# Performance work log

Measured on AMD Instinct MI355X. Metric: run time of the kernel, lower is better.

## Reference

```python
import jax, jax.numpy as jnp
import numpy as np

H = 12  # num_heads

def setup_inputs() -> dict:
    key = jax.random.key(0)
    ks = jax.random.split(key, 6)
    B, L, D = 2, 2048, 768
    x = jax.random.normal(ks[0], (B, L, D), dtype=jnp.float32)
    token_sizes = jax.random.uniform(ks[1], (B, L), dtype=jnp.float32)
    attn_mask = jnp.triu(jnp.ones((L, L), dtype=bool), k=1)
    key_padding_mask = jnp.zeros((B, L), dtype=bool)
    qkv_w = jax.random.normal(ks[2], (3 * D, D), dtype=jnp.float32) * (D ** -0.5)
    qkv_b = jax.random.normal(ks[3], (3 * D,), dtype=jnp.float32) * 0.02
    proj_w = jax.random.normal(ks[4], (D, D), dtype=jnp.float32) * (D ** -0.5)
    proj_b = jax.random.normal(ks[5], (D,), dtype=jnp.float32) * 0.02
    return {"x": x, "token_sizes": token_sizes, "attn_mask": attn_mask,
            "key_padding_mask": key_padding_mask, "qkv_w": qkv_w, "qkv_b": qkv_b,
            "proj_w": proj_w, "proj_b": proj_b}

def reference(x, token_sizes, attn_mask, key_padding_mask, qkv_w, qkv_b, proj_w, proj_b):
    B, L, D = x.shape
    hd = D // H
    scale = hd ** -0.5
    qkv = (x @ qkv_w.T + qkv_b).reshape(B, L, 3, H, hd)
    qkv = jnp.transpose(qkv, (2, 0, 3, 1, 4))  # [3, B, H, L, hd]
    q, k, v = qkv[0], qkv[1], qkv[2]
    logits = jnp.einsum('bhqd,bhkd->bhqk', q, k) * scale  # [B,H,L,L]
    neg = jnp.finfo(logits.dtype).min
    logits = jnp.where(attn_mask[None, None, :, :], neg, logits)
    logits = jnp.where(key_padding_mask[:, None, None, :], neg, logits)
    logits = logits + jnp.log(jnp.clip(token_sizes, 1e-8))[:, None, None, :]
    attn = jax.nn.softmax(logits, axis=-1)
    out = jnp.einsum('bhqk,bhkd->bhqd', attn, v)
    out = jnp.transpose(out, (0, 2, 1, 3)).reshape(B, L, D)
    out = out @ proj_w.T + proj_b
    k_merge = k.mean(axis=1)  # [B, L, hd]
    return (out, k_merge)
```

## Files before the change

### kernel.cpp

```cpp
#include <hip/hip_runtime.h>
#include <hip/hip_bf16.h>

typedef unsigned short u16;
typedef __bf16 bf16x8 __attribute__((ext_vector_type(8)));
typedef float f32x4 __attribute__((ext_vector_type(4)));

#define QSCALE (0.125f * 1.44269504088896340736f)

__device__ __forceinline__ u16 f2bf(float f) {
    __hip_bfloat16 h = __float2bfloat16(f);
    return __builtin_bit_cast(u16, h);
}
__device__ __forceinline__ float bf2f(u16 u) {
    unsigned int x = ((unsigned int)u) << 16;
    return __builtin_bit_cast(float, x);
}
__device__ __forceinline__ bf16x8 ld_bf8(const u16* p) {
    uint4 u = *reinterpret_cast<const uint4*>(p);
    return __builtin_bit_cast(bf16x8, u);
}
__device__ __forceinline__ bf16x8 pack8f(f32x4 a, f32x4 b) {
    union { bf16x8 v; u16 u[8]; } r;
    #pragma unroll
    for (int i = 0; i < 4; i++) { r.u[i] = f2bf(a[i]); r.u[4+i] = f2bf(b[i]); }
    return r.v;
}
__device__ __forceinline__ bf16x8 pack8u(ushort4 a, ushort4 b) {
    union { bf16x8 v; ushort4 u[2]; } r;
    r.u[0] = a; r.u[1] = b;
    return r.v;
}

#define GLOAD_LDS16(g, l) __builtin_amdgcn_global_load_lds( \
    (const __attribute__((address_space(1))) unsigned int*)(g), \
    (__attribute__((address_space(3))) unsigned int*)(l), 16, 0, 0)

template<int N> __device__ __forceinline__ void s_wait_vmcnt() {
    if constexpr (N == 0)       asm volatile("s_waitcnt vmcnt(0)" ::: "memory");
    else if constexpr (N == 3)  asm volatile("s_waitcnt vmcnt(3)" ::: "memory");
    else if constexpr (N == 4)  asm volatile("s_waitcnt vmcnt(4)" ::: "memory");
}
__device__ __forceinline__ void s_bar() {
    __builtin_amdgcn_sched_barrier(0);
    __builtin_amdgcn_s_barrier();
    __builtin_amdgcn_sched_barrier(0);
}
__device__ __forceinline__ void s_wait_lgkm0_bar() {
    asm volatile("s_waitcnt lgkmcnt(0)" ::: "memory");
    __builtin_amdgcn_sched_barrier(0);
    __builtin_amdgcn_s_barrier();
    __builtin_amdgcn_sched_barrier(0);
}

__global__ __launch_bounds__(256) void prep_kernel(
    const float* __restrict__ x, const float* __restrict__ qkvw,
    const float* __restrict__ projw, const float* __restrict__ ts,
    const unsigned char* __restrict__ kpm,
    u16* __restrict__ Xb, u16* __restrict__ Wq, u16* __restrict__ Wp,
    float* __restrict__ tsw, u16* __restrict__ tbf, int* __restrict__ qarr)
{
    int i = blockIdx.x * 256 + threadIdx.x;
    const int XC4 = 4096 * 768 / 4;
    const int WQ4 = 2304 * 768 / 4;
    const int WP4 = 768 * 768 / 4;
    const float* src = nullptr; u16* dst = nullptr;
    if (i < XC4) { src = x; dst = Xb; }
    else {
        i -= XC4;
        if (i < WQ4) { src = qkvw; dst = Wq; }
        else {
            i -= WQ4;
            if (i < WP4) { src = projw; dst = Wp; }
            else {
                i -= WP4;
                if (i < 1024) {
                    float4 t = *(const float4*)(ts + i*4);
                    uchar4 k = *(const uchar4*)(kpm + i*4);
                    float4 r;
                    r.x = k.x ? 0.f : fmaxf(t.x, 1e-8f);
                    r.y = k.y ? 0.f : fmaxf(t.y, 1e-8f);
                    r.z = k.z ? 0.f : fmaxf(t.z, 1e-8f);
                    r.w = k.w ? 0.f : fmaxf(t.w, 1e-8f);
                    *(float4*)(tsw + i*4) = r;
                    ushort4 o;
                    o.x = f2bf(r.x); o.y = f2bf(r.y);
                    o.z = f2bf(r.z); o.w = f2bf(r.w);
                    *(ushort4*)(tbf + i*4) = o;
                    return;
                }
                i -= 1024;
                if (i < 256) qarr[i] = 0;
                return;
            }
        }
    }
    float4 v = *(const float4*)(src + i*4);
    ushort4 o;
    o.x = f2bf(v.x); o.y = f2bf(v.y); o.z = f2bf(v.z); o.w = f2bf(v.w);
    *(ushort4*)(dst + i*4) = o;
}

template<int EPI, int MI>
__global__ __launch_bounds__(256, 2) void gemm_bt(
    const u16* __restrict__ A, const u16* __restrict__ Bm,
    const float* __restrict__ bias, const float* __restrict__ tsw,
    u16* __restrict__ Qb, u16* __restrict__ Kb, u16* __restrict__ Vt,
    float* __restrict__ outp)
{
    constexpr int BM = MI * 32;
    constexpr int ACALLS = MI / 2;
    constexpr int SA = ACALLS + 2;
    constexpr int NT = 24;
    __shared__ u16 As[2][BM * 32];
    __shared__ u16 Bs[2][128 * 32];
    const int K = 768;
    const int tid = threadIdx.x;
    const int nwg = gridDim.x * gridDim.y;
    const int flat = blockIdx.y * gridDim.x + blockIdx.x;
    const int per = nwg >> 3;
    const int swz = (flat & 7) * per + (flat >> 3);
    const int m0 = (swz / gridDim.x) * BM;
    const int n0 = (swz % gridDim.x) * 128;
    const int w = tid >> 6, lane = tid & 63;
    const int wr = (w >> 1) * (MI * 16), wc = (w & 1) * 64;
    const int g = lane >> 4, l16 = lane & 15;

    const int srow = lane >> 2;
    const int scol = (lane & 3) * 8;
    const u16* gA[ACALLS];
    #pragma unroll
    for (int c = 0; c < ACALLS; c++)
        gA[c] = A + (size_t)(m0 + (c*4 + w)*16 + srow) * K + scol;
    const u16* gB[2];
    #pragma unroll
    for (int c = 0; c < 2; c++)
        gB[c] = Bm + (size_t)(n0 + (c*4 + w)*16 + srow) * K + scol;

#define GSTAGE(buf, kk) do { \
    _Pragma("unroll") \
    for (int c = 0; c < ACALLS; c++) \
        GLOAD_LDS16(gA[c] + (kk), &As[buf][(c*4 + w) * 512]); \
    _Pragma("unroll") \
    for (int c = 0; c < 2; c++) \
        GLOAD_LDS16(gB[c] + (kk), &Bs[buf][(c*4 + w) * 512]); } while (0)

    f32x4 acc[MI][4] = {};
    GSTAGE(0, 0);
    GSTAGE(1, 32);
    for (int it = 0; it < NT; it++) {
        const int k0 = it * 32;
        const int cur = it & 1;
        if (it < NT - 1) s_wait_vmcnt<SA>();
        else             s_wait_vmcnt<0>();
        s_bar();
        bf16x8 af[MI], bfr[4];
        #pragma unroll
        for (int i = 0; i < MI; i++) af[i]  = ld_bf8(&As[cur][(wr + i*16 + l16)*32 + g*8]);
        #pragma unroll
        for (int j = 0; j < 4; j++)  bfr[j] = ld_bf8(&Bs[cur][(wc + j*16 + l16)*32 + g*8]);
        s_wait_lgkm0_bar();
        if (it + 2 < NT) GSTAGE(cur, k0 + 64);
        #pragma unroll
        for (int i = 0; i < MI; i++)
            #pragma unroll
            for (int j = 0; j < 4; j++)
                acc[i][j] = __builtin_amdgcn_mfma_f32_16x16x32_bf16(af[i], bfr[j], acc[i][j], 0, 0, 0);
    }
#undef GSTAGE

    #pragma unroll
    for (int j = 0; j < 4; j++) {
        const int n = n0 + wc + j*16 + l16;
        const float bs = bias[n];
        #pragma unroll
        for (int i = 0; i < MI; i++) {
            #pragma unroll
            for (int r = 0; r < 4; r++) {
                const int m = m0 + wr + i*16 + g*4 + r;
                float v = acc[i][j][r] + bs;
                if (EPI == 0) {
                    int b = m >> 11, l = m & 2047;
                    unsigned int which = (unsigned int)n / 768u;
                    int rem = n - (int)which * 768;
                    int h = rem >> 6, d = rem & 63;
                    int bh = b * 12 + h;
                    if (which == 0)      Qb[((size_t)bh*2048 + l)*64 + d] = f2bf(v * QSCALE);
                    else if (which == 1) Kb[((size_t)bh*2048 + l)*64 + d] = f2bf(v);
                    else                 Vt[((size_t)bh*64 + d)*2048 + l] = f2bf(v * tsw[b*2048 + l]);
                } else {
                    outp[(size_t)m * 768 + n] = v;
                }
            }
        }
    }
}

__global__ __launch_bounds__(256, 3) void attn_kernel(
    const u16* __restrict__ Q, const u16* __restrict__ Kb,
    const u16* __restrict__ Vt, const u16* __restrict__ tbf,
    u16* __restrict__ O, int* __restrict__ qarr)
{
    __shared__ u16 Ks[2][64 * 64];
    __shared__ u16 Vs[2][64 * 64];
    __shared__ int s_item;
    const int tid = threadIdx.x;
    const int w = tid >> 6, lane = tid & 63;
    const int g = lane >> 4, l16 = lane & 15;
    const int sw = l16 & 7;
    const int srow = lane >> 3;
    const int sslot = (lane & 7) ^ srow;
    int xcd;
    asm("s_getreg_b32 %0, hwreg(HW_REG_XCC_ID)" : "=s"(xcd));
    xcd &= 7;

    for (;;) {
        if (tid == 0) {
            int it = -1;
            #pragma unroll 1
            for (int k2 = 0; k2 < 8; k2++) {
                const int y = (xcd + k2) & 7;
                const int i = atomicAdd(&qarr[y << 5], 1);
                if (i < 96) {
                    const int qi = i / 3;
                    it = (31 - qi) * 24 + y * 3 + (i - qi * 3);
                    break;
                }
            }
            s_item = it;
        }
        __syncthreads();
        const int item = s_item;
        if (item < 0) return;
        const int qt = item / 24;
        const int bh = item - qt * 24;
        const int b = bh / 12, h = bh - b * 12;
        const int q0 = qt * 64 + w * 16;
        const int nkt = qt + 1;

        const u16* Qp = Q + ((size_t)bh * 2048 + q0) * 64;
        const u16* Kp = Kb + (size_t)bh * 2048 * 64;
        const u16* Vp = Vt + (size_t)bh * 64 * 2048;
        const u16* tb = tbf + b * 2048;

        const u16* gK0 = Kp + (size_t)(w*16 +     srow) * 64   + sslot * 8;
        const u16* gK1 = Kp + (size_t)(w*16 + 8 + srow) * 64   + sslot * 8;
        const u16* gV0 = Vp + (size_t)(w*16 +     srow) * 2048 + sslot * 8;
        const u16* gV1 = Vp + (size_t)(w*16 + 8 + srow) * 2048 + sslot * 8;

#define ASTAGE(buf, kk) do { \
    GLOAD_LDS16(gK0 + (size_t)(kk) * 64, &Ks[buf][(w*16    ) * 64]); \
    GLOAD_LDS16(gK1 + (size_t)(kk) * 64, &Ks[buf][(w*16 + 8) * 64]); \
    GLOAD_LDS16(gV0 + (kk),              &Vs[buf][(w*16    ) * 64]); \
    GLOAD_LDS16(gV1 + (kk),              &Vs[buf][(w*16 + 8) * 64]); } while (0)

        const bf16x8 qf0 = ld_bf8(Qp + l16 * 64 + g * 8);
        const bf16x8 qf1 = ld_bf8(Qp + l16 * 64 + 32 + g * 8);

        ushort4 tc0, tc1, tc2, tc3;
        { const u16* tp = tb + 4*g;
          tc0 = *(const ushort4*)(tp);      tc1 = *(const ushort4*)(tp + 16);
          tc2 = *(const ushort4*)(tp + 32); tc3 = *(const ushort4*)(tp + 48); }
        ASTAGE(0, 0);

        f32x4 o[4] = {};
        f32x4 lpacc = {};
        float m = -1e30f;
        const int qmy = q0 + l16;

        __syncthreads();

        for (int kt = 0; kt < nkt; kt++) {
            const int cur = kt & 1;
            const int k0 = kt * 64;

            ushort4 tn0 = tc0, tn1 = tc1, tn2 = tc2, tn3 = tc3;
            if (kt + 1 < nkt) {
                const u16* tp = tb + k0 + 64 + 4*g;
                tn0 = *(const ushort4*)(tp);      tn1 = *(const ushort4*)(tp + 16);
                tn2 = *(const ushort4*)(tp + 32); tn3 = *(const ushort4*)(tp + 48);
                ASTAGE(cur ^ 1, k0 + 64);
            }

            const int ko0 = 8 * (g ^ sw);
            bf16x8 kf[4][2];
            #pragma unroll
            for (int t = 0; t < 4; t++) {
                const u16* kb = &Ks[cur][(t*16 + l16) * 64];
                kf[t][0] = ld_bf8(kb + ko0);
                kf[t][1] = ld_bf8(kb + (ko0 ^ 32));
            }
            const int gh = g >> 1, gl = 4 * (g & 1);
            ushort4 va[4][4];
            #pragma unroll
            for (int j = 0; j < 4; j++) {
                const u16* vb = &Vs[cur][(j*16 + l16) * 64];
                va[j][0] = *(const ushort4*)(vb + (((0 + gh) ^ sw) << 3) + gl);
                va[j][1] = *(const ushort4*)(vb + (((2 + gh) ^ sw) << 3) + gl);
                va[j][2] = *(const ushort4*)(vb + (((4 + gh) ^ sw) << 3) + gl);
                va[j][3] = *(const ushort4*)(vb + (((6 + gh) ^ sw) << 3) + gl);
            }

            f32x4 s[4];
            #pragma unroll
            for (int t = 0; t < 4; t++) {
                f32x4 z = {};
                z = __builtin_amdgcn_mfma_f32_16x16x32_bf16(kf[t][0], qf0, z, 0, 0, 0);
                z = __builtin_amdgcn_mfma_f32_16x16x32_bf16(kf[t][1], qf1, z, 0, 0, 0);
                s[t] = z;
            }
            if (kt == qt) {
                #pragma unroll
                for (int t = 0; t < 4; t++)
                    #pragma unroll
                    for (int r = 0; r < 4; r++) {
                        const int key = k0 + t*16 + 4*g + r;
                        if (key > qmy) s[t][r] = -1e30f;
                    }
            }
            float pmax = -1e30f;
            #pragma unroll
            for (int t = 0; t < 4; t++)
                #pragma unroll
                for (int r = 0; r < 4; r++)
                    pmax = fmaxf(pmax, s[t][r]);
            pmax = fmaxf(pmax, __shfl_xor(pmax, 16));
            pmax = fmaxf(pmax, __shfl_xor(pmax, 32));
            if (!__all(pmax <= m + 8.f)) {
                const float mn = fmaxf(m, pmax);
                const float sc = __builtin_amdgcn_exp2f(m - mn);
                m = mn;
                #pragma unroll
                for (int r = 0; r < 4; r++) {
                    const float scr = __shfl(sc, (lane & 48) + 4*g + r);
                    o[0][r] *= scr; o[1][r] *= scr; o[2][r] *= scr; o[3][r] *= scr;
                    lpacc[r] *= scr;
                }
            }
            #pragma unroll
            for (int t = 0; t < 4; t++)
                #pragma unroll
                for (int r = 0; r < 4; r++)
                    s[t][r] = __builtin_amdgcn_exp2f(s[t][r] - m);
            const bf16x8 pa01 = pack8f(s[0], s[1]);
            const bf16x8 pa23 = pack8f(s[2], s[3]);
            __builtin_amdgcn_s_setprio(1);
            lpacc = __builtin_amdgcn_mfma_f32_16x16x32_bf16(pa01, pack8u(tc0, tc1), lpacc, 0, 0, 0);
            lpacc = __builtin_amdgcn_mfma_f32_16x16x32_bf16(pa23, pack8u(tc2, tc3), lpacc, 0, 0, 0);
            #pragma unroll
            for (int j = 0; j < 4; j++) {
                o[j] = __builtin_amdgcn_mfma_f32_16x16x32_bf16(pa01, pack8u(va[j][0], va[j][1]), o[j], 0, 0, 0);
                o[j] = __builtin_amdgcn_mfma_f32_16x16x32_bf16(pa23, pack8u(va[j][2], va[j][3]), o[j], 0, 0, 0);
            }
            __builtin_amdgcn_s_setprio(0);
            __syncthreads();
            tc0 = tn0; tc1 = tn1; tc2 = tn2; tc3 = tn3;
        }
#undef ASTAGE

        float rlr[4];
        #pragma unroll
        for (int r = 0; r < 4; r++) rlr[r] = 1.f / lpacc[r];
        #pragma unroll
        for (int j = 0; j < 4; j++)
            #pragma unroll
            for (int r = 0; r < 4; r++) {
                const int q = q0 + 4*g + r;
                O[((size_t)b*2048 + q)*768 + h*64 + j*16 + l16] = f2bf(o[j][r] * rlr[r]);
            }
        __syncthreads();
    }
}

__global__ __launch_bounds__(256) void kmerge_kernel(
    const u16* __restrict__ Kb, float* __restrict__ out)
{
    const int idx = blockIdx.x * 256 + threadIdx.x;
    const int d4 = (idx & 15) * 4;
    const int l = (idx >> 4) & 2047;
    const int b = idx >> 15;
    float4 acc = {0.f, 0.f, 0.f, 0.f};
    #pragma unroll
    for (int h = 0; h < 12; h++) {
        ushort4 v = *(const ushort4*)&Kb[(((size_t)(b*12 + h))*2048 + l)*64 + d4];
        acc.x += bf2f(v.x); acc.y += bf2f(v.y);
        acc.z += bf2f(v.z); acc.w += bf2f(v.w);
    }
    const float s = 1.f / 12.f;
    float4 r = {acc.x * s, acc.y * s, acc.z * s, acc.w * s};
    *(float4*)&out[(((size_t)b*2048 + l))*64 + d4] = r;
}

extern "C" void kernel_launch(void* const* d_in, const int* in_sizes, int n_in,
                              void* d_out, int out_size, void* d_ws, size_t ws_size,
                              hipStream_t stream)
{
    const float* x     = (const float*)d_in[0];
    const float* ts    = (const float*)d_in[1];
    const unsigned char* kpm = (const unsigned char*)d_in[3];
    const float* qkvw  = (const float*)d_in[4];
    const float* qkvb  = (const float*)d_in[5];
    const float* projw = (const float*)d_in[6];
    const float* projb = (const float*)d_in[7];
    float* out = (float*)d_out;

    char* ws = (char*)d_ws;
    u16* Xb = (u16*)ws;  ws += (size_t)4096 * 768 * 2;
    u16* Wq = (u16*)ws;  ws += (size_t)2304 * 768 * 2;
    u16* Wp = (u16*)ws;  ws += (size_t)768 * 768 * 2;
    u16* Qb = (u16*)ws;  ws += (size_t)24 * 2048 * 64 * 2;
    u16* Kb = (u16*)ws;  ws += (size_t)24 * 2048 * 64 * 2;
    u16* Vt = (u16*)ws;  ws += (size_t)24 * 2048 * 64 * 2;
    u16* Ob = (u16*)ws;  ws += (size_t)4096 * 768 * 2;
    float* tsw = (float*)ws;  ws += (size_t)2 * 2048 * 4;
    u16* tbf = (u16*)ws;  ws += (size_t)2 * 2048 * 2;
    int* qarr = (int*)ws;

    const int prep4 = (4096*768 + 2304*768 + 768*768) / 4 + 1024 + 256;
    prep_kernel<<<(prep4 + 255) / 256, 256, 0, stream>>>(
        x, qkvw, projw, ts, kpm, Xb, Wq, Wp, tsw, tbf, qarr);

    gemm_bt<0, 4><<<dim3(18, 32), 256, 0, stream>>>(Xb, Wq, qkvb, tsw, Qb, Kb, Vt, nullptr);

    attn_kernel<<<dim3(768), 256, 0, stream>>>(Qb, Kb, Vt, tbf, Ob, qarr);

    kmerge_kernel<<<(2*2048*16) / 256, 256, 0, stream>>>(Kb, out + 3145728);

    gemm_bt<1, 2><<<dim3(6, 64), 256, 0, stream>>>(Ob, Wp, projb, nullptr, nullptr, nullptr, nullptr, out);
}
```

Before: 110.9 us.

## Load K/V tiles directly from global memory instead of double-buffered LDS

Removes the LDS double-buffer staging of K and V tiles in the attention kernel. Each wave now reads its K and V fragments straight from global memory, relying on L2/L1 caching, and the per-iteration block barrier is dropped. Occupancy bound changes from 3 to 2 and the persistent grid shrinks from 768 to 512 blocks. This removes LDS traffic and synchronisation, but the four waves of a block now each fetch the same K/V data redundantly and the prefetch overlap is lost.

```diff
diff --git a/kernel.cpp b/kernel.cpp
--- a/kernel.cpp
+++ b/kernel.cpp
@@ -195,25 +195,21 @@
     }
 }
 
-__global__ __launch_bounds__(256, 3) void attn_kernel(
+__global__ __launch_bounds__(256, 2) void attn_kernel(
     const u16* __restrict__ Q, const u16* __restrict__ Kb,
     const u16* __restrict__ Vt, const u16* __restrict__ tbf,
     u16* __restrict__ O, int* __restrict__ qarr)
 {
-    __shared__ u16 Ks[2][64 * 64];
-    __shared__ u16 Vs[2][64 * 64];
     __shared__ int s_item;
     const int tid = threadIdx.x;
     const int w = tid >> 6, lane = tid & 63;
     const int g = lane >> 4, l16 = lane & 15;
-    const int sw = l16 & 7;
-    const int srow = lane >> 3;
-    const int sslot = (lane & 7) ^ srow;
     int xcd;
     asm("s_getreg_b32 %0, hwreg(HW_REG_XCC_ID)" : "=s"(xcd));
     xcd &= 7;
 
     for (;;) {
+        __syncthreads();
         if (tid == 0) {
             int it = -1;
             #pragma unroll 1
@@ -242,63 +238,37 @@
         const u16* Vp = Vt + (size_t)bh * 64 * 2048;
         const u16* tb = tbf + b * 2048;
 
-        const u16* gK0 = Kp + (size_t)(w*16 +     srow) * 64   + sslot * 8;
-        const u16* gK1 = Kp + (size_t)(w*16 + 8 + srow) * 64   + sslot * 8;
-        const u16* gV0 = Vp + (size_t)(w*16 +     srow) * 2048 + sslot * 8;
-        const u16* gV1 = Vp + (size_t)(w*16 + 8 + srow) * 2048 + sslot * 8;
-
-#define ASTAGE(buf, kk) do { \
-    GLOAD_LDS16(gK0 + (size_t)(kk) * 64, &Ks[buf][(w*16    ) * 64]); \
-    GLOAD_LDS16(gK1 + (size_t)(kk) * 64, &Ks[buf][(w*16 + 8) * 64]); \
-    GLOAD_LDS16(gV0 + (kk),              &Vs[buf][(w*16    ) * 64]); \
-    GLOAD_LDS16(gV1 + (kk),              &Vs[buf][(w*16 + 8) * 64]); } while (0)
-
         const bf16x8 qf0 = ld_bf8(Qp + l16 * 64 + g * 8);
         const bf16x8 qf1 = ld_bf8(Qp + l16 * 64 + 32 + g * 8);
-
-        ushort4 tc0, tc1, tc2, tc3;
-        { const u16* tp = tb + 4*g;
-          tc0 = *(const ushort4*)(tp);      tc1 = *(const ushort4*)(tp + 16);
-          tc2 = *(const ushort4*)(tp + 32); tc3 = *(const ushort4*)(tp + 48); }
-        ASTAGE(0, 0);
 
         f32x4 o[4] = {};
         f32x4 lpacc = {};
         float m = -1e30f;
         const int qmy = q0 + l16;
 
-        __syncthreads();
-
         for (int kt = 0; kt < nkt; kt++) {
-            const int cur = kt & 1;
             const int k0 = kt * 64;
 
-            ushort4 tn0 = tc0, tn1 = tc1, tn2 = tc2, tn3 = tc3;
-            if (kt + 1 < nkt) {
-                const u16* tp = tb + k0 + 64 + 4*g;
-                tn0 = *(const ushort4*)(tp);      tn1 = *(const ushort4*)(tp + 16);
-                tn2 = *(const ushort4*)(tp + 32); tn3 = *(const ushort4*)(tp + 48);
-                ASTAGE(cur ^ 1, k0 + 64);
-            }
-
-            const int ko0 = 8 * (g ^ sw);
             bf16x8 kf[4][2];
             #pragma unroll
             for (int t = 0; t < 4; t++) {
-                const u16* kb = &Ks[cur][(t*16 + l16) * 64];
-                kf[t][0] = ld_bf8(kb + ko0);
-                kf[t][1] = ld_bf8(kb + (ko0 ^ 32));
-            }
-            const int gh = g >> 1, gl = 4 * (g & 1);
+                const u16* kp = Kp + (size_t)(k0 + t*16 + l16) * 64 + g * 8;
+                kf[t][0] = ld_bf8(kp);
+                kf[t][1] = ld_bf8(kp + 32);
+            }
             ushort4 va[4][4];
             #pragma unroll
             for (int j = 0; j < 4; j++) {
-                const u16* vb = &Vs[cur][(j*16 + l16) * 64];
-                va[j][0] = *(const ushort4*)(vb + (((0 + gh) ^ sw) << 3) + gl);
-                va[j][1] = *(const ushort4*)(vb + (((2 + gh) ^ sw) << 3) + gl);
-                va[j][2] = *(const ushort4*)(vb + (((4 + gh) ^ sw) << 3) + gl);
-                va[j][3] = *(const ushort4*)(vb + (((6 + gh) ^ sw) << 3) + gl);
-            }
+                const u16* vp = Vp + (size_t)(j*16 + l16) * 2048 + k0 + 4*g;
+                va[j][0] = *(const ushort4*)(vp);
+                va[j][1] = *(const ushort4*)(vp + 16);
+                va[j][2] = *(const ushort4*)(vp + 32);
+                va[j][3] = *(const ushort4*)(vp + 48);
+            }
+            ushort4 tc0, tc1, tc2, tc3;
+            { const u16* tp = tb + k0 + 4*g;
+              tc0 = *(const ushort4*)(tp);      tc1 = *(const ushort4*)(tp + 16);
+              tc2 = *(const ushort4*)(tp + 32); tc3 = *(const ushort4*)(tp + 48); }
 
             f32x4 s[4];
             #pragma unroll
@@ -352,10 +322,7 @@
                 o[j] = __builtin_amdgcn_mfma_f32_16x16x32_bf16(pa23, pack8u(va[j][2], va[j][3]), o[j], 0, 0, 0);
             }
             __builtin_amdgcn_s_setprio(0);
-            __syncthreads();
-            tc0 = tn0; tc1 = tn1; tc2 = tn2; tc3 = tn3;
         }
-#undef ASTAGE
 
         float rlr[4];
         #pragma unroll
@@ -367,7 +334,6 @@
                 const int q = q0 + 4*g + r;
                 O[((size_t)b*2048 + q)*768 + h*64 + j*16 + l16] = f2bf(o[j][r] * rlr[r]);
             }
-        __syncthreads();
     }
 }
 
@@ -421,7 +387,7 @@
 
     gemm_bt<0, 4><<<dim3(18, 32), 256, 0, stream>>>(Xb, Wq, qkvb, tsw, Qb, Kb, Vt, nullptr);
 
-    attn_kernel<<<dim3(768), 256, 0, stream>>>(Qb, Kb, Vt, tbf, Ob, qarr);
+    attn_kernel<<<dim3(512), 256, 0, stream>>>(Qb, Kb, Vt, tbf, Ob, qarr);
 
     kmerge_kernel<<<(2*2048*16) / 256, 256, 0, stream>>>(Kb, out + 3145728);
 
```

Result: slower. 224.4 us (+102.4%).

## Triple-buffer attention K/V tiles with one barrier per step and a global work queue

Applied to the files above, without the earlier changes.

Expands the K/V LDS ring from two to three buffers. It replaces the trailing per-iteration __syncthreads with one vmcnt-gated barrier at the start of each step. The XCD-local atomic work queues become a single global counter, and the persistent grid and occupancy hint drop to 2 blocks per CU (512 blocks). The aim is to cut barrier stalls and overlap loads better, at the cost of more LDS per block, lower occupancy and loss of XCD L2 locality.

```diff
diff --git a/kernel.cpp b/kernel.cpp
--- a/kernel.cpp
+++ b/kernel.cpp
@@ -39,6 +39,7 @@
     if constexpr (N == 0)       asm volatile("s_waitcnt vmcnt(0)" ::: "memory");
     else if constexpr (N == 3)  asm volatile("s_waitcnt vmcnt(3)" ::: "memory");
     else if constexpr (N == 4)  asm volatile("s_waitcnt vmcnt(4)" ::: "memory");
+    else if constexpr (N == 8)  asm volatile("s_waitcnt vmcnt(8)" ::: "memory");
 }
 __device__ __forceinline__ void s_bar() {
     __builtin_amdgcn_sched_barrier(0);
@@ -195,13 +196,13 @@
     }
 }
 
-__global__ __launch_bounds__(256, 3) void attn_kernel(
+__global__ __launch_bounds__(256, 2) void attn_kernel(
     const u16* __restrict__ Q, const u16* __restrict__ Kb,
     const u16* __restrict__ Vt, const u16* __restrict__ tbf,
     u16* __restrict__ O, int* __restrict__ qarr)
 {
-    __shared__ u16 Ks[2][64 * 64];
-    __shared__ u16 Vs[2][64 * 64];
+    __shared__ u16 Ks[3][64 * 64];
+    __shared__ u16 Vs[3][64 * 64];
     __shared__ int s_item;
     const int tid = threadIdx.x;
     const int w = tid >> 6, lane = tid & 63;
@@ -209,30 +210,18 @@
     const int sw = l16 & 7;
     const int srow = lane >> 3;
     const int sslot = (lane & 7) ^ srow;
-    int xcd;
-    asm("s_getreg_b32 %0, hwreg(HW_REG_XCC_ID)" : "=s"(xcd));
-    xcd &= 7;
 
     for (;;) {
+        __syncthreads();
         if (tid == 0) {
-            int it = -1;
-            #pragma unroll 1
-            for (int k2 = 0; k2 < 8; k2++) {
-                const int y = (xcd + k2) & 7;
-                const int i = atomicAdd(&qarr[y << 5], 1);
-                if (i < 96) {
-                    const int qi = i / 3;
-                    it = (31 - qi) * 24 + y * 3 + (i - qi * 3);
-                    break;
-                }
-            }
-            s_item = it;
+            const int i = atomicAdd(&qarr[0], 1);
+            s_item = (i < 768) ? i : -1;
         }
         __syncthreads();
         const int item = s_item;
         if (item < 0) return;
-        const int qt = item / 24;
-        const int bh = item - qt * 24;
+        const int qt = 31 - (item / 24);
+        const int bh = item - (item / 24) * 24;
         const int b = bh / 12, h = bh - b * 12;
         const int q0 = qt * 64 + w * 16;
         const int nkt = qt + 1;
@@ -267,19 +256,22 @@
         float m = -1e30f;
         const int qmy = q0 + l16;
 
-        __syncthreads();
-
+        int cur = 0;
         for (int kt = 0; kt < nkt; kt++) {
-            const int cur = kt & 1;
             const int k0 = kt * 64;
+            const int nxt = (cur == 2) ? 0 : cur + 1;
 
             ushort4 tn0 = tc0, tn1 = tc1, tn2 = tc2, tn3 = tc3;
             if (kt + 1 < nkt) {
                 const u16* tp = tb + k0 + 64 + 4*g;
                 tn0 = *(const ushort4*)(tp);      tn1 = *(const ushort4*)(tp + 16);
                 tn2 = *(const ushort4*)(tp + 32); tn3 = *(const ushort4*)(tp + 48);
-                ASTAGE(cur ^ 1, k0 + 64);
-            }
+                ASTAGE(nxt, k0 + 64);
+                s_wait_vmcnt<8>();
+            } else {
+                s_wait_vmcnt<0>();
+            }
+            s_bar();
 
             const int ko0 = 8 * (g ^ sw);
             bf16x8 kf[4][2];
@@ -352,8 +344,8 @@
                 o[j] = __builtin_amdgcn_mfma_f32_16x16x32_bf16(pa23, pack8u(va[j][2], va[j][3]), o[j], 0, 0, 0);
             }
             __builtin_amdgcn_s_setprio(0);
-            __syncthreads();
             tc0 = tn0; tc1 = tn1; tc2 = tn2; tc3 = tn3;
+            cur = nxt;
         }
 #undef ASTAGE
 
@@ -367,7 +359,6 @@
                 const int q = q0 + 4*g + r;
                 O[((size_t)b*2048 + q)*768 + h*64 + j*16 + l16] = f2bf(o[j][r] * rlr[r]);
             }
-        __syncthreads();
     }
 }
 
@@ -421,7 +412,7 @@
 
     gemm_bt<0, 4><<<dim3(18, 32), 256, 0, stream>>>(Xb, Wq, qkvb, tsw, Qb, Kb, Vt, nullptr);
 
-    attn_kernel<<<dim3(768), 256, 0, stream>>>(Qb, Kb, Vt, tbf, Ob, qarr);
+    attn_kernel<<<dim3(512), 256, 0, stream>>>(Qb, Kb, Vt, tbf, Ob, qarr);
 
     kmerge_kernel<<<(2*2048*16) / 256, 256, 0, stream>>>(Kb, out + 3145728);
 
```

After: 106.0 us. 1.05x faster.
